# Performance work log

Measured on AMD Instinct MI355X. Metric: run time of the kernel, lower is better.

Reference implementation:

```python
import jax, jax.numpy as jnp
import numpy as np

N = 8192        # number of nodes
F_IN = 64       # input feature dim
F_HID = 64      # hidden feature dim
F_OUT = 16      # output (class) dim
EDGE_P = 0.002  # ~16 avg degree


def setup_inputs() -> dict:
    key = jax.random.key(0)
    k1, k2, k3, k4 = jax.random.split(key, 4)
    # sparse-ish binary adjacency stored dense (matches module's dense/sparse adj tensor)
    adj = jax.random.bernoulli(k1, EDGE_P, (N, N)).astype(jnp.float32)
    H = jax.random.normal(k2, (N, F_IN), dtype=jnp.float32)
    W1 = jax.random.normal(k3, (F_IN, F_HID), dtype=jnp.float32) * 0.1
    W2 = jax.random.normal(k4, (F_HID, F_OUT), dtype=jnp.float32) * 0.1
    return {"H": H, "adj": adj, "W1": W1, "W2": W2}


def _normalize(adj):
    # D^{-1/2} (A + I) D^{-1/2}, done once at init in the torch module
    n = adj.shape[0]
    a_hat = adj + jnp.eye(n, dtype=adj.dtype)
    deg = jnp.sum(a_hat, axis=1)
    d_inv_sqrt = jnp.where(deg > 0, jax.lax.rsqrt(deg), 0.0)
    return a_hat * d_inv_sqrt[:, None] * d_inv_sqrt[None, :]


def reference(H, adj, W1, W2):
    A = _normalize(adj)
    # layer 1: aggregate-then-transform + ReLU
    H1 = jax.nn.relu(A @ (H @ W1))      # [N, F_HID]
    # layer 2 (last): softmax over classes
    H2 = A @ (H1 @ W2)                  # [N, F_OUT]
    return jax.nn.softmax(H2, axis=-1)
```

## Files before the change

kernel.cpp:

```cpp
#include <hip/hip_runtime.h>

#define N 8192
#define CAP 64

__global__ __launch_bounds__(256) void k_scan(const float* __restrict__ adj,
                                              float* __restrict__ dinv,
                                              int* __restrict__ rowcnt,
                                              int* __restrict__ colidx) {
    __shared__ int cnt;
    const int row = blockIdx.x;
    if (threadIdx.x == 0) cnt = 0;
    __syncthreads();
    const float4* r = (const float4*)(adj + (size_t)row * N);
    int* ci = colidx + (size_t)row * CAP;
#pragma unroll
    for (int it = 0; it < 8; ++it) {
        const int i4 = it * 256 + threadIdx.x;
        const float4 v = r[i4];
        const int e0 = i4 * 4;
        if (v.x != 0.f) { int s = atomicAdd(&cnt, 1); if (s < CAP) ci[s] = e0;     }
        if (v.y != 0.f) { int s = atomicAdd(&cnt, 1); if (s < CAP) ci[s] = e0 + 1; }
        if (v.z != 0.f) { int s = atomicAdd(&cnt, 1); if (s < CAP) ci[s] = e0 + 2; }
        if (v.w != 0.f) { int s = atomicAdd(&cnt, 1); if (s < CAP) ci[s] = e0 + 3; }
    }
    __syncthreads();
    if (threadIdx.x == 0) {
        const int c = cnt;
        rowcnt[row] = c < CAP ? c : CAP;
        dinv[row] = rsqrtf((float)c + 1.0f);
    }
}

__global__ __launch_bounds__(256) void k_xw1(const float* __restrict__ H,
                                             const float* __restrict__ W1,
                                             float* __restrict__ X) {
    __shared__ float w[64][64];
    const int t = threadIdx.x;
    for (int i = t; i < 4096; i += 256) w[i >> 6][i & 63] = W1[i];
    __syncthreads();
    const int wave = t >> 6, lane = t & 63;
#pragma unroll
    for (int rr = 0; rr < 8; ++rr) {
        const int row = blockIdx.x * 32 + wave * 8 + rr;
        const float h = H[row * 64 + lane];
        float acc = 0.f;
#pragma unroll
        for (int k = 0; k < 64; ++k) {
            const float hk = __shfl(h, k, 64);
            acc += hk * w[k][lane];
        }
        X[row * 64 + lane] = acc;
    }
}

__global__ __launch_bounds__(256) void k_agg1(const float* __restrict__ X,
                                              const float* __restrict__ dinv,
                                              const int* __restrict__ rowcnt,
                                              const int* __restrict__ colidx,
                                              const float* __restrict__ W2,
                                              float* __restrict__ Y) {
    __shared__ float w2[64][16];
    const int t = threadIdx.x;
    for (int i = t; i < 1024; i += 256) w2[i >> 4][i & 15] = W2[i];
    __syncthreads();
    const int wave = t >> 6, lane = t & 63;
    const int row = blockIdx.x * 4 + wave;
    const float di = dinv[row];
    float acc = di * X[row * 64 + lane];
    const int cnt = rowcnt[row];
    const int* ci = colidx + (size_t)row * CAP;
    for (int k = 0; k < cnt; ++k) {
        const int j = ci[k];
        acc += dinv[j] * X[j * 64 + lane];
    }
    float h1 = di * acc;
    h1 = h1 > 0.f ? h1 : 0.f;
    float y = 0.f;
#pragma unroll
    for (int k = 0; k < 64; ++k) {
        const float hk = __shfl(h1, k, 64);
        y += hk * w2[k][lane & 15];
    }
    if (lane < 16) Y[row * 16 + lane] = y;
}

__global__ __launch_bounds__(256) void k_agg2(const float* __restrict__ Y,
                                              const float* __restrict__ dinv,
                                              const int* __restrict__ rowcnt,
                                              const int* __restrict__ colidx,
                                              float* __restrict__ out) {
    const int t = threadIdx.x;
    const int wave = t >> 6, lane = t & 63;
    const int row = blockIdx.x * 4 + wave;
    const int c = lane & 15;
    const float di = dinv[row];
    float acc = di * Y[row * 16 + c];
    const int cnt = rowcnt[row];
    const int* ci = colidx + (size_t)row * CAP;
    for (int k = 0; k < cnt; ++k) {
        const int j = ci[k];
        acc += dinv[j] * Y[j * 16 + c];
    }
    const float h2 = di * acc;
    float m = h2;
#pragma unroll
    for (int off = 1; off < 16; off <<= 1) m = fmaxf(m, __shfl_xor(m, off, 16));
    const float e = __expf(h2 - m);
    float s = e;
#pragma unroll
    for (int off = 1; off < 16; off <<= 1) s += __shfl_xor(s, off, 16);
    if (lane < 16) out[row * 16 + lane] = e / s;
}

extern "C" void kernel_launch(void* const* d_in, const int* in_sizes, int n_in,
                              void* d_out, int out_size, void* d_ws, size_t ws_size,
                              hipStream_t stream) {
    const float* H   = (const float*)d_in[0];
    const float* adj = (const float*)d_in[1];
    const float* W1  = (const float*)d_in[2];
    const float* W2  = (const float*)d_in[3];
    float* out = (float*)d_out;

    char* w = (char*)d_ws;
    float* dinv   = (float*)(w);
    int*   rowcnt = (int*)(w + 32 * 1024);
    int*   colidx = (int*)(w + 64 * 1024);
    float* X      = (float*)(w + 64 * 1024 + (size_t)N * CAP * 4);
    float* Y      = (float*)(w + 64 * 1024 + (size_t)N * CAP * 4
                               + (size_t)N * 64 * 4);

    k_scan<<<dim3(N),      dim3(256), 0, stream>>>(adj, dinv, rowcnt, colidx);
    k_xw1 <<<dim3(N / 32), dim3(256), 0, stream>>>(H, W1, X);
    k_agg1<<<dim3(N / 4),  dim3(256), 0, stream>>>(X, dinv, rowcnt, colidx, W2, Y);
    k_agg2<<<dim3(N / 4),  dim3(256), 0, stream>>>(Y, dinv, rowcnt, colidx, out);
}
```

Measured before the change: 406.4 us.

## Batch scan atomics, nontemporal adjacency loads, split neighbor aggregation across waves

The scan kernel now loads the adjacency as integer vectors with nontemporal hints and reserves slots with one atomic per nonzero quad instead of one per nonzero element. Layer-1 aggregation uses one block per row, with four waves each summing a strided subset of neighbors and combining partials through shared memory. Layer-2 aggregation splits each row's neighbor list over the four 16-lane groups and reduces them with shuffles. The scan over the dense 256MB adjacency likely dominates runtime, so the gains from the aggregation changes are uncertain, and the layer-1 kernel now launches four times as many blocks.

```diff
diff --git a/kernel.cpp b/kernel.cpp
--- a/kernel.cpp
+++ b/kernel.cpp
@@ -2,6 +2,9 @@
 
 #define N 8192
 #define CAP 64
+
+typedef unsigned int u32;
+typedef u32 u32x4 __attribute__((ext_vector_type(4)));
 
 __global__ __launch_bounds__(256) void k_scan(const float* __restrict__ adj,
                                               float* __restrict__ dinv,
@@ -11,17 +14,21 @@
     const int row = blockIdx.x;
     if (threadIdx.x == 0) cnt = 0;
     __syncthreads();
-    const float4* r = (const float4*)(adj + (size_t)row * N);
+    const u32x4* r = (const u32x4*)(adj + (size_t)row * N);
     int* ci = colidx + (size_t)row * CAP;
 #pragma unroll
     for (int it = 0; it < 8; ++it) {
         const int i4 = it * 256 + threadIdx.x;
-        const float4 v = r[i4];
-        const int e0 = i4 * 4;
-        if (v.x != 0.f) { int s = atomicAdd(&cnt, 1); if (s < CAP) ci[s] = e0;     }
-        if (v.y != 0.f) { int s = atomicAdd(&cnt, 1); if (s < CAP) ci[s] = e0 + 1; }
-        if (v.z != 0.f) { int s = atomicAdd(&cnt, 1); if (s < CAP) ci[s] = e0 + 2; }
-        if (v.w != 0.f) { int s = atomicAdd(&cnt, 1); if (s < CAP) ci[s] = e0 + 3; }
+        const u32x4 v = __builtin_nontemporal_load(&r[i4]);
+        const int m = (v.x ? 1 : 0) | (v.y ? 2 : 0) | (v.z ? 4 : 0) | (v.w ? 8 : 0);
+        if (m) {
+            const int e0 = i4 * 4;
+            int s = atomicAdd(&cnt, __popc(m));
+            if (m & 1) { if (s < CAP) ci[s] = e0;     ++s; }
+            if (m & 2) { if (s < CAP) ci[s] = e0 + 1; ++s; }
+            if (m & 4) { if (s < CAP) ci[s] = e0 + 2; ++s; }
+            if (m & 8) { if (s < CAP) ci[s] = e0 + 3; ++s; }
+        }
     }
     __syncthreads();
     if (threadIdx.x == 0) {
@@ -60,28 +67,30 @@
                                               const float* __restrict__ W2,
                                               float* __restrict__ Y) {
     __shared__ float w2[64][16];
+    __shared__ float part[3][64];
     const int t = threadIdx.x;
     for (int i = t; i < 1024; i += 256) w2[i >> 4][i & 15] = W2[i];
-    __syncthreads();
     const int wave = t >> 6, lane = t & 63;
-    const int row = blockIdx.x * 4 + wave;
-    const float di = dinv[row];
-    float acc = di * X[row * 64 + lane];
+    const int row = blockIdx.x;
     const int cnt = rowcnt[row];
     const int* ci = colidx + (size_t)row * CAP;
-    for (int k = 0; k < cnt; ++k) {
+    float acc = 0.f;
+    for (int k = wave; k < cnt; k += 4) {
         const int j = ci[k];
-        acc += dinv[j] * X[j * 64 + lane];
+        acc += dinv[j] * X[(size_t)j * 64 + lane];
     }
-    float h1 = di * acc;
-    h1 = h1 > 0.f ? h1 : 0.f;
-    float y = 0.f;
+    const float di = dinv[row];
+    if (wave == 0) acc += di * X[(size_t)row * 64 + lane];
+    else part[wave - 1][lane] = acc;
+    __syncthreads();
+    if (wave == 0) {
+        float h1 = di * (acc + part[0][lane] + part[1][lane] + part[2][lane]);
+        h1 = fmaxf(h1, 0.f);
+        float y = 0.f;
 #pragma unroll
-    for (int k = 0; k < 64; ++k) {
-        const float hk = __shfl(h1, k, 64);
-        y += hk * w2[k][lane & 15];
+        for (int k = 0; k < 64; ++k) y += __shfl(h1, k, 64) * w2[k][lane & 15];
+        if (lane < 16) Y[row * 16 + lane] = y;
     }
-    if (lane < 16) Y[row * 16 + lane] = y;
 }
 
 __global__ __launch_bounds__(256) void k_agg2(const float* __restrict__ Y,
@@ -92,15 +101,18 @@
     const int t = threadIdx.x;
     const int wave = t >> 6, lane = t & 63;
     const int row = blockIdx.x * 4 + wave;
-    const int c = lane & 15;
-    const float di = dinv[row];
-    float acc = di * Y[row * 16 + c];
+    const int g = lane >> 4, c = lane & 15;
     const int cnt = rowcnt[row];
     const int* ci = colidx + (size_t)row * CAP;
-    for (int k = 0; k < cnt; ++k) {
+    float acc = 0.f;
+    for (int k = g; k < cnt; k += 4) {
         const int j = ci[k];
         acc += dinv[j] * Y[j * 16 + c];
     }
+    const float di = dinv[row];
+    if (g == 0) acc += di * Y[row * 16 + c];
+    acc += __shfl_xor(acc, 32, 64);
+    acc += __shfl_xor(acc, 16, 64);
     const float h2 = di * acc;
     float m = h2;
 #pragma unroll
@@ -131,6 +143,6 @@
 
     k_scan<<<dim3(N),      dim3(256), 0, stream>>>(adj, dinv, rowcnt, colidx);
     k_xw1 <<<dim3(N / 32), dim3(256), 0, stream>>>(H, W1, X);
-    k_agg1<<<dim3(N / 4),  dim3(256), 0, stream>>>(X, dinv, rowcnt, colidx, W2, Y);
+    k_agg1<<<dim3(N),      dim3(256), 0, stream>>>(X, dinv, rowcnt, colidx, W2, Y);
     k_agg2<<<dim3(N / 4),  dim3(256), 0, stream>>>(Y, dinv, rowcnt, colidx, out);
 }
```

Result: faster. 377.4 us (-7.1%).
